# Performance work log

Measured on AMD Instinct MI355X. Metric: run time of the kernel, lower is better.

Reference implementation:

```python
import jax, jax.numpy as jnp
import numpy as np

B, S, D, H = 2, 2048, 1024, 16
HW = D // H  # head width = 64
MASK_FILL = -100000000.0


def setup_inputs() -> dict:
    key0 = jax.random.key(0)
    ks = jax.random.split(key0, 12)
    inp = {
        "query": jax.random.normal(ks[0], (B, S, D), jnp.float32),
        "key": jax.random.normal(ks[1], (B, S, D), jnp.float32),
        "value": jax.random.normal(ks[2], (B, S, D), jnp.float32),
        # bool mask, True masks; broadcasts over batch and heads
        "mask": jax.random.randint(ks[3], (S, S), 0, 2).astype(jnp.bool_),
        # per-head projection kernels: (heads, head_width, d_in)
        "Wq": jax.random.normal(ks[4], (H, HW, D), jnp.float32) * 0.02,
        "bq": jnp.zeros((H, HW), jnp.float32),
        "Wk": jax.random.normal(ks[5], (H, HW, D), jnp.float32) * 0.02,
        "bk": jnp.zeros((H, HW), jnp.float32),
        "Wv": jax.random.normal(ks[6], (H, HW, D), jnp.float32) * 0.02,
        "bv": jnp.zeros((H, HW), jnp.float32),
        # collapse projector: contracts (heads, head_width) -> d_output
        "Wo": jax.random.normal(ks[7], (D, H, HW), jnp.float32) * 0.02,
        "bo": jnp.zeros((D,), jnp.float32),
    }
    return inp


def reference(query, key, value, mask, Wq, bq, Wk, bk, Wv, bv, Wo, bo):
    # head projections -> (b, h, s, w)
    q = jnp.einsum("bsd,hwd->bhsw", query, Wq) + bq[:, None, :]
    k = jnp.einsum("btd,hwd->bhtw", key, Wk) + bk[:, None, :]
    v = jnp.einsum("btd,hwd->bhtw", value, Wv) + bv[:, None, :]
    # unscaled logits, masked_fill, softmax (matches original exactly)
    logits = jnp.einsum("bhsw,bhtw->bhst", q, k)
    logits = jnp.where(mask, MASK_FILL, logits)
    score = jax.nn.softmax(logits, axis=-1)
    # NOTE: original divides AV output by sqrt(head_width) AFTER softmax
    attn = jnp.einsum("bhst,bhtw->bhsw", score, v) / jnp.sqrt(jnp.float32(HW))
    # collapse heads -> (b, s, d_output)
    out = jnp.einsum("bhsw,ohw->bso", attn, Wo) + bo
    return out
```

## Files before the change

kernel.cpp:

```cpp
#include <hip/hip_runtime.h>
#include <hip/hip_bf16.h>
#include <math.h>

#define S_LEN   2048
#define D_MODEL 1024
#define N_HEADS 16
#define HEAD_W  64
#define BATCH   2
#define MROWS   (BATCH * S_LEN)
#define MASK_FILL -100000000.0f
#define LOG2E 1.4426950408889634f

typedef __attribute__((ext_vector_type(8))) short bf16x8;
typedef __attribute__((ext_vector_type(4))) float f32x4;
typedef __attribute__((ext_vector_type(16))) float f32x16;
typedef unsigned short u16;
typedef unsigned int   u32;
typedef unsigned long long u64;

__device__ __forceinline__ float fast_exp2(float x) {
#if __has_builtin(__builtin_amdgcn_exp2f)
    return __builtin_amdgcn_exp2f(x);
#else
    return __builtin_exp2f(x);
#endif
}

__device__ __forceinline__ float fast_rcp(float x) {
#if __has_builtin(__builtin_amdgcn_rcpf)
    return __builtin_amdgcn_rcpf(x);
#else
    return 1.0f / x;
#endif
}

__device__ __forceinline__ u16 f2bf(float f) {
    u32 u = __float_as_uint(f);
    return (u16)((u + 0x7fffu + ((u >> 16) & 1u)) >> 16);
}

__device__ __forceinline__ u32 pack_bf16x2(float lo, float hi) {
    __hip_bfloat162 t = __float22bfloat162_rn(make_float2(lo, hi));
    u32 r;
    __builtin_memcpy(&r, &t, 4);
    return r;
}

__device__ __forceinline__ void gld_lds16(const void* gp, void* lp) {
    __builtin_amdgcn_global_load_lds(
        (const __attribute__((address_space(1))) u32*)gp,
        (__attribute__((address_space(3))) u32*)lp, 16, 0, 0);
}

__device__ __forceinline__ float maskz(float p, u64 w) {
    float r;
    asm("v_cndmask_b32 %0, %1, 0, %2" : "=v"(r) : "v"(p), "s"(w));
    return r;
}

struct CvtJobs {
    const float* src[7];
    u16* dst[7];
    int n[7];
};
__global__ __launch_bounds__(256) void prep_kernel(
    CvtJobs j, const unsigned char* __restrict__ mask, u64* __restrict__ bits) {
    const int t = blockIdx.y;
    if (t < 7) {
        const float* s = j.src[t];
        u16* d = j.dst[t];
        const int n = j.n[t];
        int i = (blockIdx.x * 256 + threadIdx.x) * 4;
        if (i < n) {
            float4 v = *(const float4*)(s + i);
            ushort4 o;
            o.x = f2bf(v.x); o.y = f2bf(v.y); o.z = f2bf(v.z); o.w = f2bf(v.w);
            *(ushort4*)(d + i) = o;
        }
        return;
    }
    if (blockIdx.x >= 2048) return;
    __shared__ int isByte;
    if (threadIdx.x == 0) isByte = 0;
    __syncthreads();
    const int e0 = blockIdx.x * 2048;
    const uint2 v = ((const uint2*)(mask + e0))[threadIdx.x];
    if (((v.x | v.y) & 0xFFFFFF00u) != 0u) isByte = 1;
    __syncthreads();
    const int ib = isByte;
    const int* mi = (const int*)mask;
#pragma unroll
    for (int jj = 0; jj < 8; ++jj) {
        const int e = e0 + jj * 256 + threadIdx.x;
        const bool m = ib ? (mask[e] != 0) : (mi[e] != 0);
        const u64 bl = __ballot(m);
        if ((e & 63) == 0) bits[e >> 6] = bl;
    }
}

__global__ __launch_bounds__(256) void maskt_kernel(
    const u64* __restrict__ bits, u64* __restrict__ words) {
    const int tid = threadIdx.x, wv = tid >> 6, ln = tid & 63;
    const int l31 = ln & 31, hi = ln >> 5;
    const int sg = blockIdx.x;
#pragma unroll
    for (int ci = 0; ci < 8; ++ci) {
        const int c = wv * 8 + ci;
        const u64 rw = bits[(size_t)(sg * 32 + l31) * 32 + c];
        u64 keep = 0;
#pragma unroll
        for (int k = 0; k < 32; ++k) {
            const int T = k >> 4, g = (k >> 2) & 3, q = k & 3;
            const bool m = ((rw >> (T * 32 + q + 8 * g + 4 * hi)) & 1ull) != 0ull;
            const u64 bl = __ballot(m);
            if (ln == k) keep = bl;
        }
        if (ln < 32) words[((size_t)(sg * 32 + c) << 5) + ln] = keep;
    }
}

__device__ __forceinline__ void gemm_core_bf16(const u16* __restrict__ A,
                                               const u16* __restrict__ Bt,
                                               int m0, int n0, f32x4 acc[4][4]) {
    __shared__ u16 As[2][4096];
    __shared__ u16 Bs[2][4096];
    const int tid = threadIdx.x;
    const int wv = tid >> 6, ln = tid & 63;
    const int lane16 = ln & 15, quad = ln >> 4;
    const int wr = (wv >> 1) * 64, wc = (wv & 1) * 64;
    const u16* A0 = A + (size_t)(m0 + ln) * D_MODEL + wv * 8;
    const u16* A1 = A + (size_t)(m0 + 64 + ln) * D_MODEL + wv * 8;
    const u16* B0 = Bt + (size_t)(n0 + ln) * D_MODEL + wv * 8;
    const u16* B1 = Bt + (size_t)(n0 + 64 + ln) * D_MODEL + wv * 8;

    gld_lds16(A0, &As[0][wv * 1024]);
    gld_lds16(A1, &As[0][wv * 1024 + 512]);
    gld_lds16(B0, &Bs[0][wv * 1024]);
    gld_lds16(B1, &Bs[0][wv * 1024 + 512]);

    for (int kt = 0; kt < D_MODEL / 32; ++kt) {
        const int buf = kt & 1;
        __syncthreads();
        if (kt < D_MODEL / 32 - 1) {
            const int ko = (kt + 1) * 32;
            gld_lds16(A0 + ko, &As[buf ^ 1][wv * 1024]);
            gld_lds16(A1 + ko, &As[buf ^ 1][wv * 1024 + 512]);
            gld_lds16(B0 + ko, &Bs[buf ^ 1][wv * 1024]);
            gld_lds16(B1 + ko, &Bs[buf ^ 1][wv * 1024 + 512]);
        }
        bf16x8 af[4], bfv[4];
#pragma unroll
        for (int mt = 0; mt < 4; ++mt)
            af[mt] = *(const bf16x8*)&As[buf][quad * 1024 + (wr + mt * 16 + lane16) * 8];
#pragma unroll
        for (int nt = 0; nt < 4; ++nt)
            bfv[nt] = *(const bf16x8*)&Bs[buf][quad * 1024 + (wc + nt * 16 + lane16) * 8];
#pragma unroll
        for (int mt = 0; mt < 4; ++mt)
#pragma unroll
            for (int nt = 0; nt < 4; ++nt)
                acc[mt][nt] = __builtin_amdgcn_mfma_f32_16x16x32_bf16(
                    af[mt], bfv[nt], acc[mt][nt], 0, 0, 0);
    }
}

__global__ __launch_bounds__(256, 4) void qkv_gemm_kernel(
    const u16* __restrict__ xq, const u16* __restrict__ xk, const u16* __restrict__ xv,
    const u16* __restrict__ wq, const u16* __restrict__ wk, const u16* __restrict__ wv,
    const float* __restrict__ bq, const float* __restrict__ bk, const float* __restrict__ bv,
    u16* __restrict__ qb, u16* __restrict__ kb, u16* __restrict__ vtmp) {
    const int d = (blockIdx.z * 32 + blockIdx.y) * 8 + blockIdx.x;
    const int w0 = (d & 7) * 96 + (d >> 3);
    const int z = w0 >> 8;
    const int rem = w0 & 255;
    const int m0 = (rem >> 3) * 128, n0 = (rem & 7) * 128;
    const u16* A; const u16* Bt; const float* bias; u16* outp;
    if (z == 0)      { A = xq; Bt = wq; bias = bq; outp = qb; }
    else if (z == 1) { A = xk; Bt = wk; bias = bk; outp = kb; }
    else             { A = xv; Bt = wv; bias = bv; outp = vtmp; }
    f32x4 acc[4][4] = {};
    gemm_core_bf16(A, Bt, m0, n0, acc);

    const int tid = threadIdx.x;
    const int wvi = tid >> 6, ln = tid & 63;
    const int lane16 = ln & 15, quad = ln >> 4;
    const int wr = (wvi >> 1) * 64, wc = (wvi & 1) * 64;
    const float scale = (z == 0) ? LOG2E : 1.0f;
#pragma unroll
    for (int nt = 0; nt < 4; ++nt) {
        const int n = n0 + wc + nt * 16 + lane16;
        const float bb = bias[n];
        const int h = n >> 6, w = n & 63;
#pragma unroll
        for (int mt = 0; mt < 4; ++mt)
#pragma unroll
            for (int r = 0; r < 4; ++r) {
                const int m = m0 + wr + mt * 16 + quad * 4 + r;
                const int bidx = m >> 11, s = m & 2047;
                outp[((size_t)((bidx * N_HEADS + h) * S_LEN + s)) * HEAD_W + w] =
                    f2bf((acc[mt][nt][r] + bb) * scale);
            }
    }
}

__global__ __launch_bounds__(256) void vtrans_kernel(
    const u16* __restrict__ vtmp, u16* __restrict__ vbt) {
    __shared__ u16 T[64][72];
    const int tid = threadIdx.x;
    const int bh = blockIdx.y;
    const int s0 = blockIdx.x * 64;
    const int row = tid >> 2, seg = (tid & 3) * 16;
    const u16* src = vtmp + ((size_t)bh * S_LEN + s0 + row) * HEAD_W + seg;
    uint4 a = *(const uint4*)src;
    uint4 b2 = *(const uint4*)(src + 8);
    u16 tmp[16];
    *(uint4*)tmp = a; *(uint4*)(tmp + 8) = b2;
#pragma unroll
    for (int j = 0; j < 16; ++j) T[seg + j][row] = tmp[j];
    __syncthreads();
    u16* dst = vbt + ((size_t)bh * HEAD_W + row) * S_LEN + s0 + seg;
    *(uint4*)dst       = *(const uint4*)&T[row][seg];
    *(uint4*)(dst + 8) = *(const uint4*)&T[row][seg + 8];
}

__global__ __launch_bounds__(256, 4) void out_gemm_kernel(
    const u16* __restrict__ ab, const u16* __restrict__ wo,
    const float* __restrict__ bo, float* __restrict__ out) {
    const int d = blockIdx.y * 8 + blockIdx.x;
    const int w0 = (d & 7) * 32 + (d >> 3);
    const int m0 = (w0 >> 3) * 128, n0 = (w0 & 7) * 128;
    f32x4 acc[4][4] = {};
    gemm_core_bf16(ab, wo, m0, n0, acc);
    const int tid = threadIdx.x;
    const int wvi = tid >> 6, ln = tid & 63;
    const int lane16 = ln & 15, quad = ln >> 4;
    const int wr = (wvi >> 1) * 64, wc = (wvi & 1) * 64;
#pragma unroll
    for (int nt = 0; nt < 4; ++nt) {
        const int n = n0 + wc + nt * 16 + lane16;
        const float bb = bo[n];
#pragma unroll
        for (int mt = 0; mt < 4; ++mt)
#pragma unroll
            for (int r = 0; r < 4; ++r) {
                const int m = m0 + wr + mt * 16 + quad * 4 + r;
                out[(size_t)m * D_MODEL + n] = acc[mt][nt][r] + bb;
            }
    }
}

__global__ __launch_bounds__(512, 4) void attn_kernel(
    const u16* __restrict__ qbuf, const u16* __restrict__ kbuf,
    const u16* __restrict__ vbt, const u64* __restrict__ maskw,
    float* __restrict__ Opart, float* __restrict__ lpart) {
    __shared__ u16 Ks[2][4096];
    __shared__ u16 Vt[2][4096];
    __shared__ u16 Ps[8][32 * 72];
    const int tid = threadIdx.x;
    const int wv = tid >> 6, ln = tid & 63;
    const int l31 = ln & 31, hi = ln >> 5;
    const int lid = (blockIdx.z * N_HEADS + blockIdx.y) * 8 + blockIdx.x;
    const int nid = (lid & 7) * 64 + (lid >> 3);
    const int s_idx = nid & 7;
    const int G = nid >> 3;
    const int h = G & 15;
    const int bz = G >> 4;
    const int b = bz >> 1, hf = bz & 1;
    const int s_blk = s_idx * 256;
    const int c0 = hf * 16;
    const size_t hb = ((size_t)(b * N_HEADS + h)) * S_LEN * HEAD_W;
    const u16* Qg = qbuf + hb;
    const u16* Kg = kbuf + hb;
    const u16* Vg = vbt + hb;
    const int sgw = (s_blk >> 5) + wv;

    bf16x8 qa2[4];
#pragma unroll
    for (int ks = 0; ks < 4; ++ks)
        qa2[ks] = *(const bf16x8*)(Qg +
            (size_t)(s_blk + wv * 32 + l31) * HEAD_W + ks * 16 + hi * 8);

    {
        const int t0g = c0 * 64;
        gld_lds16(Kg + (size_t)(t0g + ln) * HEAD_W + wv * 8, &Ks[0][wv * 512]);
        gld_lds16(Vg + (size_t)ln * S_LEN + t0g + wv * 8, &Vt[0][wv * 512]);
    }

    f32x16 oacc2[2] = {};
    float lsum = 0.0f;

    for (int ci = 0; ci < 16; ++ci) {
        const int c = c0 + ci;
        const int buf = ci & 1;
        __syncthreads();
        if (ci < 15) {
            const int t1 = (c + 1) * 64;
            gld_lds16(Kg + (size_t)(t1 + ln) * HEAD_W + wv * 8, &Ks[buf ^ 1][wv * 512]);
            gld_lds16(Vg + (size_t)ln * S_LEN + t1 + wv * 8, &Vt[buf ^ 1][wv * 512]);
        }

#pragma unroll
        for (int T = 0; T < 2; ++T) {
            f32x16 st = {};
#pragma unroll
            for (int ks = 0; ks < 4; ++ks) {
                const bf16x8 kf = *(const bf16x8*)&Ks[buf][
                    (ks * 2 + hi) * 512 + (T * 32 + l31) * 8];
                st = __builtin_amdgcn_mfma_f32_32x32x16_bf16(
                    kf, qa2[ks], st, 0, 0, 0);
            }
            const u64* __restrict__ wp = maskw +
                __builtin_amdgcn_readfirstlane(((sgw * 32 + c) << 5) + T * 16);
#pragma unroll
            for (int g = 0; g < 4; ++g) {
                const float p0 = maskz(fast_exp2(st[4 * g + 0]), wp[4 * g + 0]);
                const float p1 = maskz(fast_exp2(st[4 * g + 1]), wp[4 * g + 1]);
                const float p2 = maskz(fast_exp2(st[4 * g + 2]), wp[4 * g + 2]);
                const float p3 = maskz(fast_exp2(st[4 * g + 3]), wp[4 * g + 3]);
                lsum += (p0 + p1) + (p2 + p3);
                uint2 pk;
                pk.x = pack_bf16x2(p0, p1);
                pk.y = pack_bf16x2(p2, p3);
                *(uint2*)&Ps[wv][l31 * 72 + T * 32 + 8 * g + 4 * hi] = pk;
            }
        }

#pragma unroll
        for (int T = 0; T < 2; ++T)
#pragma unroll
            for (int gg = 0; gg < 2; ++gg) {
                const bf16x8 pf = *(const bf16x8*)&Ps[wv][
                    l31 * 72 + T * 32 + gg * 16 + hi * 8];
#pragma unroll
                for (int W = 0; W < 2; ++W) {
                    const bf16x8 vf = *(const bf16x8*)&Vt[buf][
                        (T * 4 + gg * 2 + hi) * 512 + (W * 32 + l31) * 8];
                    oacc2[W] = __builtin_amdgcn_mfma_f32_32x32x16_bf16(
                        pf, vf, oacc2[W], 0, 0, 0);
                }
            }
    }

    float* OpB = Opart + ((size_t)(hf * 4096 + b * 2048)) * 1024;
#pragma unroll
    for (int W = 0; W < 2; ++W)
#pragma unroll
        for (int r = 0; r < 16; ++r) {
            const int s = s_blk + wv * 32 + (r & 3) + 8 * (r >> 2) + 4 * hi;
            OpB[(size_t)s * 1024 + h * 64 + W * 32 + l31] = oacc2[W][r];
        }
    lsum += __shfl_xor(lsum, 32);
    if (ln < 32) {
        const int srow = s_blk + wv * 32 + ln;
        lpart[(size_t)(hf * 4096 + b * 2048 + srow) * 16 + h] = lsum;
    }
}

__global__ __launch_bounds__(256) void combine_kernel(
    const float* __restrict__ Op, const float* __restrict__ lp,
    u16* __restrict__ ab) {
    const int idx4 = blockIdx.x * 256 + threadIdx.x;
    const int row = idx4 >> 8;
    const int d = (idx4 & 255) * 4;
    const int h = d >> 6;
    const float l = lp[(size_t)row * 16 + h] + lp[(size_t)(4096 + row) * 16 + h];
    const float inv = 0.125f * fast_rcp(l);
    float4 a = *(const float4*)(Op + (size_t)row * 1024 + d);
    float4 b = *(const float4*)(Op + (size_t)(4096 + row) * 1024 + d);
    ushort4 o;
    o.x = f2bf((a.x + b.x) * inv);
    o.y = f2bf((a.y + b.y) * inv);
    o.z = f2bf((a.z + b.z) * inv);
    o.w = f2bf((a.w + b.w) * inv);
    *(ushort4*)(ab + (size_t)row * 1024 + d) = o;
}

extern "C" void kernel_launch(void* const* d_in, const int* in_sizes, int n_in,
                              void* d_out, int out_size, void* d_ws, size_t ws_size,
                              hipStream_t stream) {
    const float* query = (const float*)d_in[0];
    const float* key   = (const float*)d_in[1];
    const float* value = (const float*)d_in[2];
    const void*  mask  = d_in[3];
    const float* Wq = (const float*)d_in[4];
    const float* bq = (const float*)d_in[5];
    const float* Wk = (const float*)d_in[6];
    const float* bk = (const float*)d_in[7];
    const float* Wv = (const float*)d_in[8];
    const float* bv = (const float*)d_in[9];
    const float* Wo = (const float*)d_in[10];
    const float* bo = (const float*)d_in[11];
    float* out = (float*)d_out;

    char* ws = (char*)d_ws;
    const size_t MB = 1024 * 1024;
    u64* bits  = (u64*)ws;
    u64* maskt = (u64*)(ws + 512 * 1024);
    u16* wob  = (u16*)(ws + 1 * MB);
    u16* qb   = (u16*)(ws + 3 * MB);
    u16* kb   = (u16*)(ws + 11 * MB);
    u16* vbt  = (u16*)(ws + 19 * MB);
    char* uA = ws + 27 * MB;
    u16* xq   = (u16*)(uA);
    u16* xk   = (u16*)(uA + 8 * MB);
    u16* xv   = (u16*)(uA + 16 * MB);
    u16* wqb  = (u16*)(uA + 24 * MB);
    u16* wkb  = (u16*)(uA + 26 * MB);
    u16* wvb  = (u16*)(uA + 28 * MB);
    u16* vtmp = (u16*)(uA + 30 * MB);
    float* Opart = (float*)(uA);
    float* lpart = (float*)(uA + 32 * MB);
    u16* ab = qb;

    const size_t NACT = (size_t)MROWS * D_MODEL;
    const size_t NW   = (size_t)D_MODEL * D_MODEL;

    CvtJobs j;
    j.src[0] = query; j.dst[0] = xq;  j.n[0] = (int)NACT;
    j.src[1] = key;   j.dst[1] = xk;  j.n[1] = (int)NACT;
    j.src[2] = value; j.dst[2] = xv;  j.n[2] = (int)NACT;
    j.src[3] = Wq;    j.dst[3] = wqb; j.n[3] = (int)NW;
    j.src[4] = Wk;    j.dst[4] = wkb; j.n[4] = (int)NW;
    j.src[5] = Wv;    j.dst[5] = wvb; j.n[5] = (int)NW;
    j.src[6] = Wo;    j.dst[6] = wob; j.n[6] = (int)NW;
    prep_kernel<<<dim3(NACT / 1024, 8), 256, 0, stream>>>(
        j, (const unsigned char*)mask, bits);
    maskt_kernel<<<dim3(64), 256, 0, stream>>>(bits, maskt);

    qkv_gemm_kernel<<<dim3(D_MODEL / 128, MROWS / 128, 3), 256, 0, stream>>>(
        xq, xk, xv, wqb, wkb, wvb, bq, bk, bv, qb, kb, vtmp);
    vtrans_kernel<<<dim3(S_LEN / 64, BATCH * N_HEADS), 256, 0, stream>>>(vtmp, vbt);
    attn_kernel<<<dim3(8, N_HEADS, 4), 512, 0, stream>>>(
        qb, kb, vbt, maskt, Opart, lpart);
    combine_kernel<<<4096, 256, 0, stream>>>(Opart, lpart, ab);
    out_gemm_kernel<<<dim3(D_MODEL / 128, MROWS / 128), 256, 0, stream>>>(
        ab, wob, bo, out);
}
```

Baseline: 286.8 us.

## Drop split-KV attention and fuse normalization into attention epilogue

The attention kernel no longer splits the key sequence into two halves. Each block now walks all 32 key chunks and normalizes its own output by the row sum, then writes bf16 directly. This removes the fp32 partial-output round trip through memory and the separate combine kernel launch. In exchange the grid shrinks from 512 to 256 blocks with twice the serial loop length, so GPU occupancy and parallelism drop.

```diff
diff --git a/kernel.cpp b/kernel.cpp
--- a/kernel.cpp
+++ b/kernel.cpp
@@ -252,7 +252,7 @@
 __global__ __launch_bounds__(512, 4) void attn_kernel(
     const u16* __restrict__ qbuf, const u16* __restrict__ kbuf,
     const u16* __restrict__ vbt, const u64* __restrict__ maskw,
-    float* __restrict__ Opart, float* __restrict__ lpart) {
+    u16* __restrict__ ab) {
     __shared__ u16 Ks[2][4096];
     __shared__ u16 Vt[2][4096];
     __shared__ u16 Ps[8][32 * 72];
@@ -260,14 +260,12 @@
     const int wv = tid >> 6, ln = tid & 63;
     const int l31 = ln & 31, hi = ln >> 5;
     const int lid = (blockIdx.z * N_HEADS + blockIdx.y) * 8 + blockIdx.x;
-    const int nid = (lid & 7) * 64 + (lid >> 3);
+    const int nid = (lid & 7) * 32 + (lid >> 3);
     const int s_idx = nid & 7;
     const int G = nid >> 3;
     const int h = G & 15;
-    const int bz = G >> 4;
-    const int b = bz >> 1, hf = bz & 1;
+    const int b = G >> 4;
     const int s_blk = s_idx * 256;
-    const int c0 = hf * 16;
     const size_t hb = ((size_t)(b * N_HEADS + h)) * S_LEN * HEAD_W;
     const u16* Qg = qbuf + hb;
     const u16* Kg = kbuf + hb;
@@ -281,19 +279,17 @@
             (size_t)(s_blk + wv * 32 + l31) * HEAD_W + ks * 16 + hi * 8);
 
     {
-        const int t0g = c0 * 64;
-        gld_lds16(Kg + (size_t)(t0g + ln) * HEAD_W + wv * 8, &Ks[0][wv * 512]);
-        gld_lds16(Vg + (size_t)ln * S_LEN + t0g + wv * 8, &Vt[0][wv * 512]);
+        gld_lds16(Kg + (size_t)ln * HEAD_W + wv * 8, &Ks[0][wv * 512]);
+        gld_lds16(Vg + (size_t)ln * S_LEN + wv * 8, &Vt[0][wv * 512]);
     }
 
     f32x16 oacc2[2] = {};
     float lsum = 0.0f;
 
-    for (int ci = 0; ci < 16; ++ci) {
-        const int c = c0 + ci;
-        const int buf = ci & 1;
+    for (int c = 0; c < 32; ++c) {
+        const int buf = c & 1;
         __syncthreads();
-        if (ci < 15) {
+        if (c < 31) {
             const int t1 = (c + 1) * 64;
             gld_lds16(Kg + (size_t)(t1 + ln) * HEAD_W + wv * 8, &Ks[buf ^ 1][wv * 512]);
             gld_lds16(Vg + (size_t)ln * S_LEN + t1 + wv * 8, &Vt[buf ^ 1][wv * 512]);
@@ -341,38 +337,17 @@
             }
     }
 
-    float* OpB = Opart + ((size_t)(hf * 4096 + b * 2048)) * 1024;
-#pragma unroll
-    for (int W = 0; W < 2; ++W)
-#pragma unroll
-        for (int r = 0; r < 16; ++r) {
-            const int s = s_blk + wv * 32 + (r & 3) + 8 * (r >> 2) + 4 * hi;
-            OpB[(size_t)s * 1024 + h * 64 + W * 32 + l31] = oacc2[W][r];
-        }
     lsum += __shfl_xor(lsum, 32);
-    if (ln < 32) {
-        const int srow = s_blk + wv * 32 + ln;
-        lpart[(size_t)(hf * 4096 + b * 2048 + srow) * 16 + h] = lsum;
-    }
-}
-
-__global__ __launch_bounds__(256) void combine_kernel(
-    const float* __restrict__ Op, const float* __restrict__ lp,
-    u16* __restrict__ ab) {
-    const int idx4 = blockIdx.x * 256 + threadIdx.x;
-    const int row = idx4 >> 8;
-    const int d = (idx4 & 255) * 4;
-    const int h = d >> 6;
-    const float l = lp[(size_t)row * 16 + h] + lp[(size_t)(4096 + row) * 16 + h];
-    const float inv = 0.125f * fast_rcp(l);
-    float4 a = *(const float4*)(Op + (size_t)row * 1024 + d);
-    float4 b = *(const float4*)(Op + (size_t)(4096 + row) * 1024 + d);
-    ushort4 o;
-    o.x = f2bf((a.x + b.x) * inv);
-    o.y = f2bf((a.y + b.y) * inv);
-    o.z = f2bf((a.z + b.z) * inv);
-    o.w = f2bf((a.w + b.w) * inv);
-    *(ushort4*)(ab + (size_t)row * 1024 + d) = o;
+    u16* abB = ab + (size_t)(b * 2048) * 1024 + h * 64;
+#pragma unroll
+    for (int r = 0; r < 16; ++r) {
+        const int rho = (r & 3) + 8 * (r >> 2) + 4 * hi;
+        const float invr = 0.125f * fast_rcp(__shfl(lsum, rho));
+        const int s = s_blk + wv * 32 + rho;
+#pragma unroll
+        for (int W = 0; W < 2; ++W)
+            abB[(size_t)s * 1024 + W * 32 + l31] = f2bf(oacc2[W][r] * invr);
+    }
 }
 
 extern "C" void kernel_launch(void* const* d_in, const int* in_sizes, int n_in,
@@ -408,9 +383,7 @@
     u16* wkb  = (u16*)(uA + 26 * MB);
     u16* wvb  = (u16*)(uA + 28 * MB);
     u16* vtmp = (u16*)(uA + 30 * MB);
-    float* Opart = (float*)(uA);
-    float* lpart = (float*)(uA + 32 * MB);
-    u16* ab = qb;
+    u16* ab   = (u16*)(uA);
 
     const size_t NACT = (size_t)MROWS * D_MODEL;
     const size_t NW   = (size_t)D_MODEL * D_MODEL;
@@ -430,9 +403,8 @@
     qkv_gemm_kernel<<<dim3(D_MODEL / 128, MROWS / 128, 3), 256, 0, stream>>>(
         xq, xk, xv, wqb, wkb, wvb, bq, bk, bv, qb, kb, vtmp);
     vtrans_kernel<<<dim3(S_LEN / 64, BATCH * N_HEADS), 256, 0, stream>>>(vtmp, vbt);
-    attn_kernel<<<dim3(8, N_HEADS, 4), 512, 0, stream>>>(
-        qb, kb, vbt, maskt, Opart, lpart);
-    combine_kernel<<<4096, 256, 0, stream>>>(Opart, lpart, ab);
+    attn_kernel<<<dim3(8, N_HEADS, 2), 512, 0, stream>>>(
+        qb, kb, vbt, maskt, ab);
     out_gemm_kernel<<<dim3(D_MODEL / 128, MROWS / 128), 256, 0, stream>>>(
         ab, wob, bo, out);
 }
```

After: 289.1 us. No clear change (+0.8%).
